# Performance work log

Hardware: AMD Instinct MI355X
Metric: run time of the kernel (lower is better)

The kernel has to match this reference:

```python
import jax, jax.numpy as jnp
import numpy as np

H, D = 8, 16          # heads, per-head dim (hidden_channels=128)
HID = H * D
N = 200000            # movie nodes
E = 500000            # edges per metapath relation
IN = 256              # input feature dim
CLS = 3               # output classes


def setup_inputs() -> dict:
    key = jax.random.key(0)
    ks = jax.random.split(key, 13)
    return {
        "x_movie": jax.random.normal(ks[0], (N, IN), jnp.float32),
        "W_proj": jax.random.normal(ks[1], (IN, HID), jnp.float32) * 0.05,
        "b_proj": jnp.zeros((HID,), jnp.float32),
        "att_src0": jax.random.normal(ks[2], (H, D), jnp.float32) * 0.1,
        "att_dst0": jax.random.normal(ks[3], (H, D), jnp.float32) * 0.1,
        "att_src1": jax.random.normal(ks[4], (H, D), jnp.float32) * 0.1,
        "att_dst1": jax.random.normal(ks[5], (H, D), jnp.float32) * 0.1,
        "q": jax.random.normal(ks[6], (HID,), jnp.float32) * 0.1,
        "k_w": jax.random.normal(ks[7], (HID, HID), jnp.float32) * 0.05,
        "k_b": jnp.zeros((HID,), jnp.float32),
        "lin_w": jax.random.normal(ks[8], (HID, CLS), jnp.float32) * 0.05,
        "lin_b": jnp.zeros((CLS,), jnp.float32),
        "e0_src": jax.random.randint(ks[9], (E,), 0, N, jnp.int32),
        "e0_dst": jax.random.randint(ks[10], (E,), 0, N, jnp.int32),
        "e1_src": jax.random.randint(ks[11], (E,), 0, N, jnp.int32),
        "e1_dst": jax.random.randint(ks[12], (E,), 0, N, jnp.int32),
    }


def _han_rel(h, att_s, att_d, src, dst, n):
    # h: [N, H, D]; GAT-style per-relation attention with segment softmax over dst
    a_s = jnp.sum(h * att_s, axis=-1)                      # [N, H]
    a_d = jnp.sum(h * att_d, axis=-1)                      # [N, H]
    alpha = jax.nn.leaky_relu(a_s[src] + a_d[dst], 0.2)    # [E, H]
    m = jax.ops.segment_max(alpha, dst, num_segments=n)    # per-dst max
    ex = jnp.exp(alpha - m[dst])
    den = jax.ops.segment_sum(ex, dst, num_segments=n)
    w = ex / (den[dst] + 1e-16)                            # edge softmax (PyG eps)
    msg = (h[src] * w[:, :, None]).reshape(-1, HID)        # [E, HID]
    return jax.nn.relu(jax.ops.segment_sum(msg, dst, num_segments=n))


def reference(x_movie, W_proj, b_proj, att_src0, att_dst0, att_src1, att_dst1,
              q, k_w, k_b, lin_w, lin_b, e0_src, e0_dst, e1_src, e1_dst):
    # node-type projection (HANConv.proj), dropout omitted (eval mode)
    h = (x_movie @ W_proj + b_proj).reshape(-1, H, D)      # [N, H, D]
    out0 = _han_rel(h, att_src0, att_dst0, e0_src, e0_dst, N)  # [N, HID]
    out1 = _han_rel(h, att_src1, att_dst1, e1_src, e1_dst, N)
    # semantic-level attention (HANConv.group)
    outs = jnp.stack([out0, out1])                         # [M=2, N, HID]
    score = jnp.sum(jnp.tanh(outs @ k_w + k_b).mean(axis=1) * q, axis=-1)  # [M]
    beta = jax.nn.softmax(score)
    fused = jnp.einsum('m,mnf->nf', beta, outs)            # [N, HID]
    return fused @ lin_w + lin_b                           # [N, CLS]
```

## Files before the change

kernel.cpp:

```cpp
#include <hip/hip_runtime.h>


typedef __attribute__((ext_vector_type(8))) short bf16x8;
typedef __attribute__((ext_vector_type(4))) float f32x4;
typedef __attribute__((ext_vector_type(8))) unsigned short ushort8;

__device__ __forceinline__ unsigned short f2b(float f) {
  union { float f; unsigned u; } v; v.f = f;
  unsigned r = v.u + 0x7fffu + ((v.u >> 16) & 1u);
  return (unsigned short)(r >> 16);
}
__device__ __forceinline__ float b2f(unsigned short u) {
  union { unsigned u; float f; } v; v.u = ((unsigned)u) << 16;
  return v.f;
}
__device__ __forceinline__ float fast_tanh(float x) {
  x = fminf(fmaxf(x, -15.f), 15.f);
  float t = __expf(2.f * x);
  return 1.f - 2.f / (t + 1.f);
}
__device__ __forceinline__ void gload_lds16(const void* g, void* l) {
  __builtin_amdgcn_global_load_lds(
      (const __attribute__((address_space(1))) unsigned int*)g,
      (__attribute__((address_space(3))) unsigned int*)l, 16, 0, 0);
}

__global__ __launch_bounds__(256) void prep_lite(
    const int* __restrict__ e0d, const int* __restrict__ e1d,
    int* __restrict__ deg, int ne, int n,
    const float* __restrict__ Wp, const float* __restrict__ kwm,
    unsigned short* __restrict__ Wpf, unsigned short* __restrict__ Kwf) {
  const int tid = threadIdx.x;
  int b = blockIdx.x;
  const int cb = (2 * ne + 255) >> 8;
  if (b < cb) {
    int e = b * 256 + tid;
    if (e < ne) atomicAdd(&deg[e0d[e]], 1);
    else if (e < 2 * ne) atomicAdd(&deg[n + e1d[e - ne]], 1);
    return;
  }
  b -= cb;
  int t = b * 256 + tid;
  const float* W; unsigned short* Wf; int idx;
  if (t < 4096) { W = Wp; Wf = Wpf; idx = t; }
  else if (t < 6144) { W = kwm; Wf = Kwf; idx = t - 4096; }
  else return;
  int lane = idx & 63, nt = (idx >> 6) & 7, kt = idx >> 9;
  int c = lane & 15, ks = lane >> 4;
  int kbase = kt * 32 + ks * 8;
  int col = nt * 16 + c;
  ushort8 o;
#pragma unroll
  for (int j = 0; j < 8; ++j) o[j] = f2b(W[(size_t)(kbase + j) * 128 + col]);
  *(ushort8*)(Wf + (size_t)idx * 8) = o;
}

__global__ __launch_bounds__(256) void proj_mfma(
    const float* __restrict__ X, const unsigned short* __restrict__ Wf,
    const float* __restrict__ bias,
    const float* __restrict__ as0v, const float* __restrict__ ad0v,
    const float* __restrict__ as1v, const float* __restrict__ ad1v,
    unsigned short* __restrict__ Hb, float* __restrict__ preb, int n) {
  __shared__ float buf[2][4096];
  const int tid = threadIdx.x;
  const int wid = tid >> 6, lane = tid & 63;
  const int wm = wid >> 1, wn = wid & 1;
  const int row0 = blockIdx.x * 64;
  const int r = lane & 15, ks = lane >> 4;

  f32x4 acc[2][4] = {};
  const unsigned short* bptr = Wf + ((size_t)(wn * 4) * 64 + lane) * 8;
  bf16x8 Br0[8], Br1[8];

#define VMWAIT(N) asm volatile("s_waitcnt vmcnt(" #N ")" ::: "memory")
#define SBAR()                                                                 \
  {                                                                            \
    __builtin_amdgcn_sched_barrier(0);                                         \
    __builtin_amdgcn_s_barrier();                                              \
    __builtin_amdgcn_sched_barrier(0);                                         \
  }

#define STAGE(b, s)                                                            \
  {                                                                            \
    _Pragma("unroll")                                                          \
    for (int i = 0; i < 4; ++i) {                                              \
      int rloc = wid * 16 + i * 4 + ks;                                        \
      int grow = row0 + rloc;                                                  \
      grow = grow < n ? grow : n - 1;                                          \
      const float* src =                                                       \
          X + (size_t)grow * 256 + (s) * 64 + ((r ^ (rloc & 7)) << 2);         \
      gload_lds16(src, &buf[b][(wid * 16 + i * 4) * 64]);                      \
    }                                                                          \
  }

#define BLOAD(P, s)                                                            \
  {                                                                            \
    _Pragma("unroll")                                                          \
    for (int j = 0; j < 8; ++j)                                                \
      P[j] = *(const bf16x8*)(bptr +                                           \
                (((size_t)(s) * 2 + (j >> 2)) * 8 + (j & 3)) * 512);           \
  }

#define COMPUTE_R(b, P)                                                        \
  {                                                                            \
    _Pragma("unroll")                                                          \
    for (int kt = 0; kt < 2; ++kt) {                                           \
      bf16x8 a[2];                                                             \
      _Pragma("unroll")                                                        \
      for (int mi = 0; mi < 2; ++mi) {                                         \
        int rr = wm * 32 + mi * 16 + r;                                        \
        const float* lrow = &buf[b][rr * 64];                                  \
        int c0 = kt * 8 + ks * 2;                                              \
        int sw = rr & 7;                                                       \
        float4 f0 = *(const float4*)(lrow + ((c0 ^ sw) * 4));                  \
        float4 f1 = *(const float4*)(lrow + (((c0 + 1) ^ sw) * 4));            \
        bf16x8 v;                                                              \
        v[0] = (short)f2b(f0.x); v[1] = (short)f2b(f0.y);                      \
        v[2] = (short)f2b(f0.z); v[3] = (short)f2b(f0.w);                      \
        v[4] = (short)f2b(f1.x); v[5] = (short)f2b(f1.y);                      \
        v[6] = (short)f2b(f1.z); v[7] = (short)f2b(f1.w);                      \
        a[mi] = v;                                                             \
      }                                                                        \
      _Pragma("unroll")                                                        \
      for (int ni = 0; ni < 4; ++ni) {                                         \
        acc[0][ni] = __builtin_amdgcn_mfma_f32_16x16x32_bf16(                  \
            a[0], P[kt * 4 + ni], acc[0][ni], 0, 0, 0);                        \
        acc[1][ni] = __builtin_amdgcn_mfma_f32_16x16x32_bf16(                  \
            a[1], P[kt * 4 + ni], acc[1][ni], 0, 0, 0);                        \
      }                                                                        \
    }                                                                          \
  }

  STAGE(0, 0);
  BLOAD(Br0, 0);
  STAGE(1, 1);
  VMWAIT(4); SBAR();
  BLOAD(Br1, 1);
  COMPUTE_R(0, Br0);
  SBAR();
  STAGE(0, 2);
  VMWAIT(4); SBAR();
  BLOAD(Br0, 2);
  COMPUTE_R(1, Br1);
  SBAR();
  STAGE(1, 3);
  VMWAIT(4); SBAR();
  BLOAD(Br1, 3);
  COMPUTE_R(0, Br0);
  SBAR();
  VMWAIT(0); SBAR();
  COMPUTE_R(1, Br1);
  __syncthreads();
#undef STAGE
#undef BLOAD
#undef COMPUTE_R
#undef VMWAIT
#undef SBAR

  unsigned short* ct = (unsigned short*)&buf[0][0];
#pragma unroll
  for (int ni = 0; ni < 4; ++ni) {
    const int col = wn * 64 + ni * 16 + r;
    const float bv = bias[col];
#pragma unroll
    for (int mi = 0; mi < 2; ++mi)
#pragma unroll
      for (int i = 0; i < 4; ++i)
        ct[(wm * 32 + mi * 16 + ks * 4 + i) * 136 + col] = f2b(acc[mi][ni][i] + bv);
  }
  __syncthreads();

  {
    int row = tid >> 2, qq = tid & 3;
    int grow = row0 + row;
    if (grow < n) {
      ushort8* dst = (ushort8*)(Hb + (size_t)grow * 128 + qq * 32);
#pragma unroll
      for (int j = 0; j < 4; ++j) dst[j] = *(ushort8*)&ct[row * 136 + qq * 32 + j * 8];
    }
  }

  const size_t n8 = (size_t)n * 8;
  for (int rh = tid; rh < 512; rh += 256) {
    int row = rh >> 3, head = rh & 7;
    int node = row0 + row;
    if (node < n) {
      float hv[16];
#pragma unroll
      for (int j = 0; j < 16; ++j) hv[j] = b2f(ct[row * 136 + head * 16 + j]);
      float s0 = 0, d0 = 0, s1 = 0, d1 = 0;
      const float* p0 = as0v + head * 16;
      const float* p1 = ad0v + head * 16;
      const float* p2 = as1v + head * 16;
      const float* p3 = ad1v + head * 16;
#pragma unroll
      for (int j = 0; j < 16; ++j) {
        float v = hv[j];
        s0 += v * p0[j]; d0 += v * p1[j];
        s1 += v * p2[j]; d1 += v * p3[j];
      }
      size_t idx = (size_t)node * 8 + head;
      preb[idx] = s0;
      preb[n8 + idx] = d0;
      preb[2 * n8 + idx] = s1;
      preb[3 * n8 + idx] = d1;
    }
  }
}

__global__ __launch_bounds__(256) void scan1_kernel(
    const int* __restrict__ deg, int* __restrict__ pre, int* __restrict__ bsum, int m) {
  __shared__ int sd[256];
  int t = threadIdx.x;
  int base = blockIdx.x * 2048 + t * 8;
  int v[8], sum = 0;
#pragma unroll
  for (int j = 0; j < 8; ++j) {
    v[j] = (base + j < m) ? deg[base + j] : 0;
    sum += v[j];
  }
  sd[t] = sum;
  __syncthreads();
  for (int off = 1; off < 256; off <<= 1) {
    int x = (t >= off) ? sd[t - off] : 0;
    __syncthreads();
    if (t >= off) sd[t] += x;
    __syncthreads();
  }
  if (t == 255) bsum[blockIdx.x] = sd[255];
  int run = sd[t] - sum;
#pragma unroll
  for (int j = 0; j < 8; ++j) {
    if (base + j < m) pre[base + j] = run;
    run += v[j];
  }
}

__global__ __launch_bounds__(256) void scan2_kernel(int* __restrict__ bsum, int nb) {
  __shared__ int sd[256];
  int t = threadIdx.x;
  int v = (t < nb) ? bsum[t] : 0;
  sd[t] = v;
  __syncthreads();
  for (int off = 1; off < 256; off <<= 1) {
    int x = (t >= off) ? sd[t - off] : 0;
    __syncthreads();
    if (t >= off) sd[t] += x;
    __syncthreads();
  }
  if (t < nb) bsum[t] = sd[t] - v;
}

__global__ void scan3_kernel(int* __restrict__ pre, const int* __restrict__ bsum, int m, int total) {
  int i = blockIdx.x * 256 + threadIdx.x;
  if (i < m) pre[i] += bsum[i >> 11];
  if (i == m) pre[m] = total;
}

__global__ void fill2_kernel(const int* __restrict__ e0s, const int* __restrict__ e0d,
                             const int* __restrict__ e1s, const int* __restrict__ e1d,
                             const int* __restrict__ pre, int* __restrict__ cur,
                             int* __restrict__ csr, int ne, int n) {
  int e = blockIdx.x * 256 + threadIdx.x;
  int s, idx;
  if (e < ne) { idx = e0d[e]; s = e0s[e]; }
  else if (e < 2 * ne) { idx = n + e1d[e - ne]; s = e1s[e - ne]; }
  else return;
  int slot = pre[idx] + atomicAdd(&cur[idx], 1);
  csr[slot] = s;
}

__global__ __launch_bounds__(512) void aggscore_mfma(
    const int* __restrict__ pre, const int* __restrict__ csr,
    const unsigned short* __restrict__ Hb, const float* __restrict__ preb,
    const unsigned short* __restrict__ Kf, const float* __restrict__ kb,
    const float* __restrict__ q, const float* __restrict__ lw,
    float* __restrict__ pout, float* __restrict__ sb, int n) {
  __shared__ unsigned short at[16384];
  __shared__ float red[8];
  const int rel = blockIdx.y;
  const int tid = threadIdx.x;
  const int row0 = blockIdx.x * 128;
  const size_t n8 = (size_t)n * 8;
  const float* a_s = preb + (size_t)(2 * rel) * n8;
  const float* a_d = preb + (size_t)(2 * rel + 1) * n8;

  {
    const int lane8 = tid & 7;
    const int nsub = tid >> 3;
#pragma unroll
    for (int it = 0; it < 2; ++it) {
      int row = it * 64 + nsub;
      int node = row0 + row;
      float s = 0.f;
      float acc[16] = {};
      if (node < n) {
        int beg = pre[rel * n + node];
        int cnt = pre[rel * n + node + 1] - beg;
        if (cnt > 0) {
          float ad = a_d[(size_t)node * 8 + lane8];
          int i0 = csr[beg];
          int i1 = csr[beg + (cnt > 1 ? 1 : 0)];
          float as0 = a_s[(size_t)i0 * 8 + lane8];
          float as1 = a_s[(size_t)i1 * 8 + lane8];
          const ushort8* hp0 = (const ushort8*)(Hb + (size_t)i0 * 128 + lane8 * 16);
          const ushort8* hp1 = (const ushort8*)(Hb + (size_t)i1 * 128 + lane8 * 16);
          ushort8 h0a = hp0[0], h0b = hp0[1];
          ushort8 h1a = hp1[0], h1b = hp1[1];
          for (int k = 0; k < cnt; k += 2) {
            int c2 = (k + 2 < cnt) ? k + 2 : cnt - 1;
            int c3 = (k + 3 < cnt) ? k + 3 : cnt - 1;
            int j0 = csr[beg + c2], j1 = csr[beg + c3];
            float nas0 = a_s[(size_t)j0 * 8 + lane8];
            float nas1 = a_s[(size_t)j1 * 8 + lane8];
            const ushort8* np0 = (const ushort8*)(Hb + (size_t)j0 * 128 + lane8 * 16);
            const ushort8* np1 = (const ushort8*)(Hb + (size_t)j1 * 128 + lane8 * 16);
            ushort8 nh0a = np0[0], nh0b = np0[1];
            ushort8 nh1a = np1[0], nh1b = np1[1];
            float al0 = as0 + ad, al1 = as1 + ad;
            al0 = (al0 >= 0.f) ? al0 : 0.2f * al0;
            al1 = (al1 >= 0.f) ? al1 : 0.2f * al1;
            float p0 = __expf(al0);
            float p1 = (k + 1 < cnt) ? __expf(al1) : 0.f;
            s += p0 + p1;
#pragma unroll
            for (int j = 0; j < 8; ++j) {
              acc[j]     += p0 * b2f(h0a[j]) + p1 * b2f(h1a[j]);
              acc[8 + j] += p0 * b2f(h0b[j]) + p1 * b2f(h1b[j]);
            }
            as0 = nas0; as1 = nas1;
            h0a = nh0a; h0b = nh0b; h1a = nh1a; h1b = nh1b;
          }
        }
      }
      float inv = 1.f / (s + 1e-16f);
      ushort8 o0, o1;
#pragma unroll
      for (int j = 0; j < 8; ++j) {
        o0[j] = f2b(fmaxf(acc[j] * inv, 0.f));
        o1[j] = f2b(fmaxf(acc[8 + j] * inv, 0.f));
      }
      int sw = row & 7;
      *(ushort8*)&at[row * 128 + (((lane8 * 2) ^ sw) * 8)] = o0;
      *(ushort8*)&at[row * 128 + (((lane8 * 2 + 1) ^ sw) * 8)] = o1;
    }
  }
  __syncthreads();

  const int wid = tid >> 6;
  float part = 0.f;
  if (wid < 4) {
    const int lane = tid & 63;
    const int wm = wid >> 1, wn = wid & 1;
    const int r = lane & 15, ks = lane >> 4;
    f32x4 acc[4][4] = {};
    const unsigned short* bptr = Kf + ((size_t)(wn * 4) * 64 + lane) * 8;
    __builtin_amdgcn_s_setprio(1);
#pragma unroll
    for (int kt = 0; kt < 4; ++kt) {
      bf16x8 a[4], b[4];
#pragma unroll
      for (int mi = 0; mi < 4; ++mi) {
        int row = wm * 64 + mi * 16 + r;
        a[mi] = *(const bf16x8*)&at[row * 128 + (((kt * 4 + ks) ^ (row & 7)) * 8)];
      }
#pragma unroll
      for (int ni = 0; ni < 4; ++ni)
        b[ni] = *(const bf16x8*)(bptr + ((size_t)kt * 8 + ni) * 512);
#pragma unroll
      for (int mi = 0; mi < 4; ++mi)
#pragma unroll
        for (int ni = 0; ni < 4; ++ni)
          acc[mi][ni] = __builtin_amdgcn_mfma_f32_16x16x32_bf16(a[mi], b[ni], acc[mi][ni], 0, 0, 0);
    }
    __builtin_amdgcn_s_setprio(0);
#pragma unroll
    for (int ni = 0; ni < 4; ++ni) {
      const int col = wn * 64 + ni * 16 + r;
      const float kbv = kb[col], qv = q[col];
#pragma unroll
      for (int mi = 0; mi < 4; ++mi) {
#pragma unroll
        for (int i = 0; i < 4; ++i) {
          int row = row0 + wm * 64 + mi * 16 + ks * 4 + i;
          if (row < n) part += fast_tanh(acc[mi][ni][i] + kbv) * qv;
        }
      }
    }
  } else if (tid < 384) {
    int t2 = tid - 256;
    int node = row0 + t2;
    if (node < n) {
      float p0 = 0.f, p1 = 0.f, p2 = 0.f;
      int s = t2 & 7;
#pragma unroll
      for (int c = 0; c < 16; ++c) {
        const unsigned short* rp = &at[t2 * 128 + ((c ^ s) * 8)];
#pragma unroll
        for (int j = 0; j < 8; ++j) {
          float v = b2f(rp[j]);
          const float* w = lw + (size_t)(c * 8 + j) * 3;
          p0 += v * w[0]; p1 += v * w[1]; p2 += v * w[2];
        }
      }
      float4 o = make_float4(p0, p1, p2, 0.f);
      *(float4*)(pout + (size_t)node * 8 + rel * 4) = o;
    }
  }
#pragma unroll
  for (int off = 32; off > 0; off >>= 1) part += __shfl_down(part, off, 64);
  if ((tid & 63) == 0) red[wid] = part;
  __syncthreads();
  if (tid == 0) {
    float t = 0.f;
#pragma unroll
    for (int w = 0; w < 8; ++w) t += red[w];
    atomicAdd(&sb[rel], t);
  }
}

__global__ __launch_bounds__(256) void final3_kernel(
    const float* __restrict__ pout, const float* __restrict__ sb,
    const float* __restrict__ lb, float* __restrict__ out, int n, float invn) {
  int node = blockIdx.x * 256 + threadIdx.x;
  if (node >= n) return;
  float s0 = sb[0] * invn, s1 = sb[1] * invn;
  float m = fmaxf(s0, s1);
  float e0 = __expf(s0 - m), e1 = __expf(s1 - m);
  float d = e0 + e1;
  float b0 = e0 / d, b1 = e1 / d;
  const float4* p = (const float4*)(pout + (size_t)node * 8);
  float4 pa = p[0], pb = p[1];
  float* dd = out + (size_t)node * 3;
  dd[0] = b0 * pa.x + b1 * pb.x + lb[0];
  dd[1] = b0 * pa.y + b1 * pb.y + lb[1];
  dd[2] = b0 * pa.z + b1 * pb.z + lb[2];
}

extern "C" void kernel_launch(void* const* d_in, const int* in_sizes, int n_in,
                              void* d_out, int out_size, void* d_ws, size_t ws_size,
                              hipStream_t stream) {
  const float* x   = (const float*)d_in[0];
  const float* Wp  = (const float*)d_in[1];
  const float* bp  = (const float*)d_in[2];
  const float* as0 = (const float*)d_in[3];
  const float* ad0 = (const float*)d_in[4];
  const float* as1 = (const float*)d_in[5];
  const float* ad1 = (const float*)d_in[6];
  const float* q   = (const float*)d_in[7];
  const float* kw  = (const float*)d_in[8];
  const float* kb  = (const float*)d_in[9];
  const float* lw  = (const float*)d_in[10];
  const float* lb  = (const float*)d_in[11];
  const int* e0s = (const int*)d_in[12];
  const int* e0d = (const int*)d_in[13];
  const int* e1s = (const int*)d_in[14];
  const int* e1d = (const int*)d_in[15];
  const int n  = in_sizes[0] / 256;
  const int ne = in_sizes[12];
  float* out = (float*)d_out;

  char* ws = (char*)d_ws;
  size_t off = 0;
  auto alloc = [&](size_t b) -> char* {
    char* p = ws + off;
    off = (off + b + 255) & ~(size_t)255;
    return p;
  };
  unsigned short* h    = (unsigned short*)alloc((size_t)n * 128 * 2);
  float* preb = (float*)alloc((size_t)4 * n * 8 * 4);
  float* pout = (float*)alloc((size_t)n * 8 * 4);
  int* pre    = (int*)alloc((size_t)(2 * n + 1) * 4);
  int* csr    = (int*)alloc((size_t)2 * ne * 4);
  int* deg    = (int*)alloc(((size_t)4 * n + 4) * 4);
  int* cur    = deg + 2 * n;
  float* sb   = (float*)(deg + 4 * n);
  int* bsum   = (int*)alloc(256 * 4);
  unsigned short* Wpf = (unsigned short*)alloc((size_t)4096 * 8 * 2);
  unsigned short* Kwf = (unsigned short*)alloc((size_t)2048 * 8 * 2);

  const int m = 2 * n;
  const int nblk_scan = (m + 2047) / 2048;
  const int cnt_blks = (2 * ne + 255) / 256;

  hipMemsetAsync(deg, 0, ((size_t)4 * n + 4) * 4, stream);
  hipLaunchKernelGGL(prep_lite, dim3(cnt_blks + 24), dim3(256), 0, stream,
                     e0d, e1d, deg, ne, n, Wp, kw, Wpf, Kwf);

  const int gproj = (n + 63) / 64;
  hipLaunchKernelGGL(proj_mfma, dim3(gproj), dim3(256), 0, stream,
                     x, Wpf, bp, as0, ad0, as1, ad1, h, preb, n);

  hipLaunchKernelGGL(scan1_kernel, dim3(nblk_scan), dim3(256), 0, stream, deg, pre, bsum, m);
  hipLaunchKernelGGL(scan2_kernel, dim3(1), dim3(256), 0, stream, bsum, nblk_scan);
  hipLaunchKernelGGL(scan3_kernel, dim3((m + 1 + 255) / 256), dim3(256), 0, stream,
                     pre, bsum, m, 2 * ne);
  hipLaunchKernelGGL(fill2_kernel, dim3((2 * ne + 255) / 256), dim3(256), 0, stream,
                     e0s, e0d, e1s, e1d, pre, cur, csr, ne, n);

  hipLaunchKernelGGL(aggscore_mfma, dim3((n + 127) / 128, 2), dim3(512), 0, stream,
                     pre, csr, h, preb, Kwf, kb, q, lw, pout, sb, n);
  hipLaunchKernelGGL(final3_kernel, dim3((n + 255) / 256), dim3(256), 0, stream,
                     pout, sb, lb, out, n, 1.0f / n);
}
```

Measured before the change: 295.9 us.

## Sort destination nodes by in-degree bucket to balance aggregation work

After: 355.7 us. 1.2x slower.

```diff
diff --git a/kernel.cpp b/kernel.cpp
--- a/kernel.cpp
+++ b/kernel.cpp
@@ -53,6 +53,70 @@
 #pragma unroll
   for (int j = 0; j < 8; ++j) o[j] = f2b(W[(size_t)(kbase + j) * 128 + col]);
   *(ushort8*)(Wf + (size_t)idx * 8) = o;
+}
+
+#define NBIN 66
+__global__ __launch_bounds__(256) void hist1_kernel(
+    const int* __restrict__ deg, int* __restrict__ hist2d, int m, int n) {
+  __shared__ int lh[NBIN];
+  int tid = threadIdx.x;
+  if (tid < NBIN) lh[tid] = 0;
+  __syncthreads();
+  int base = blockIdx.x * 2048 + tid * 8;
+#pragma unroll
+  for (int j = 0; j < 8; ++j) {
+    int i = base + j;
+    if (i < m) {
+      int d = deg[i]; d = d < 32 ? d : 32;
+      atomicAdd(&lh[(i >= n ? 33 : 0) + d], 1);
+    }
+  }
+  __syncthreads();
+  if (tid < NBIN) hist2d[blockIdx.x * NBIN + tid] = lh[tid];
+}
+
+__global__ __launch_bounds__(128) void hist2_kernel(int* __restrict__ hist2d, int nb) {
+  __shared__ int tot[NBIN];
+  __shared__ int bb[NBIN];
+  int t = threadIdx.x;
+  if (t < NBIN) {
+    int run = 0;
+    for (int b = 0; b < nb; ++b) {
+      int v = hist2d[b * NBIN + t];
+      hist2d[b * NBIN + t] = run;
+      run += v;
+    }
+    tot[t] = run;
+  }
+  __syncthreads();
+  if (t == 0) {
+    int base = 0;
+    for (int j = 0; j < NBIN; ++j) { bb[j] = base; base += tot[j]; }
+  }
+  __syncthreads();
+  if (t < NBIN) {
+    int add = bb[t];
+    for (int b = 0; b < nb; ++b) hist2d[b * NBIN + t] += add;
+  }
+}
+
+__global__ __launch_bounds__(256) void scat_kernel(
+    const int* __restrict__ deg, const int* __restrict__ hist2d,
+    int* __restrict__ order, int m, int n) {
+  __shared__ int lcur[NBIN];
+  int tid = threadIdx.x;
+  if (tid < NBIN) lcur[tid] = hist2d[blockIdx.x * NBIN + tid];
+  __syncthreads();
+  int base = blockIdx.x * 2048 + tid * 8;
+#pragma unroll
+  for (int j = 0; j < 8; ++j) {
+    int i = base + j;
+    if (i < m) {
+      int d = deg[i]; d = d < 32 ? d : 32;
+      int pos = atomicAdd(&lcur[(i >= n ? 33 : 0) + d], 1);
+      order[pos] = i;
+    }
+  }
 }
 
 __global__ __launch_bounds__(256) void proj_mfma(
@@ -271,19 +335,19 @@
 }
 
 __global__ __launch_bounds__(512) void aggscore_mfma(
-    const int* __restrict__ pre, const int* __restrict__ csr,
-    const unsigned short* __restrict__ Hb, const float* __restrict__ preb,
-    const unsigned short* __restrict__ Kf, const float* __restrict__ kb,
-    const float* __restrict__ q, const float* __restrict__ lw,
-    float* __restrict__ pout, float* __restrict__ sb, int n) {
+    const int* __restrict__ order, const int* __restrict__ pre,
+    const int* __restrict__ csr, const unsigned short* __restrict__ Hb,
+    const float* __restrict__ preb, const unsigned short* __restrict__ Kf,
+    const float* __restrict__ kb, const float* __restrict__ q,
+    const float* __restrict__ lw, float* __restrict__ pout,
+    float* __restrict__ sb, int n) {
   __shared__ unsigned short at[16384];
-  __shared__ float red[8];
-  const int rel = blockIdx.y;
+  __shared__ unsigned char relw[128];
+  __shared__ float red[2][8];
   const int tid = threadIdx.x;
-  const int row0 = blockIdx.x * 128;
+  const int g0 = blockIdx.x * 128;
   const size_t n8 = (size_t)n * 8;
-  const float* a_s = preb + (size_t)(2 * rel) * n8;
-  const float* a_d = preb + (size_t)(2 * rel + 1) * n8;
+  const int m = 2 * n;
 
   {
     const int lane8 = tid & 7;
@@ -291,12 +355,18 @@
 #pragma unroll
     for (int it = 0; it < 2; ++it) {
       int row = it * 64 + nsub;
-      int node = row0 + row;
+      int g = g0 + row;
       float s = 0.f;
       float acc[16] = {};
-      if (node < n) {
-        int beg = pre[rel * n + node];
-        int cnt = pre[rel * n + node + 1] - beg;
+      if (g < m) {
+        int idx = order[g];
+        int rel = idx >= n ? 1 : 0;
+        int node = idx - rel * n;
+        if (lane8 == 0) relw[row] = (unsigned char)rel;
+        const float* a_s = preb + (size_t)(2 * rel) * n8;
+        const float* a_d = preb + (size_t)(2 * rel + 1) * n8;
+        int beg = pre[idx];
+        int cnt = pre[idx + 1] - beg;
         if (cnt > 0) {
           float ad = a_d[(size_t)node * 8 + lane8];
           int i0 = csr[beg];
@@ -332,6 +402,8 @@
             h0a = nh0a; h0b = nh0b; h1a = nh1a; h1b = nh1b;
           }
         }
+      } else if (lane8 == 0) {
+        relw[row] = 0;
       }
       float inv = 1.f / (s + 1e-16f);
       ushort8 o0, o1;
@@ -348,7 +420,7 @@
   __syncthreads();
 
   const int wid = tid >> 6;
-  float part = 0.f;
+  float part0 = 0.f, part1 = 0.f;
   if (wid < 4) {
     const int lane = tid & 63;
     const int wm = wid >> 1, wn = wid & 1;
@@ -382,15 +454,21 @@
       for (int mi = 0; mi < 4; ++mi) {
 #pragma unroll
         for (int i = 0; i < 4; ++i) {
-          int row = row0 + wm * 64 + mi * 16 + ks * 4 + i;
-          if (row < n) part += fast_tanh(acc[mi][ni][i] + kbv) * qv;
+          int row = wm * 64 + mi * 16 + ks * 4 + i;
+          if (g0 + row < m) {
+            float v = fast_tanh(acc[mi][ni][i] + kbv) * qv;
+            if (relw[row]) part1 += v; else part0 += v;
+          }
         }
       }
     }
   } else if (tid < 384) {
     int t2 = tid - 256;
-    int node = row0 + t2;
-    if (node < n) {
+    int g = g0 + t2;
+    if (g < m) {
+      int idx = order[g];
+      int rel = idx >= n ? 1 : 0;
+      int node = idx - rel * n;
       float p0 = 0.f, p1 = 0.f, p2 = 0.f;
       int s = t2 & 7;
 #pragma unroll
@@ -408,14 +486,18 @@
     }
   }
 #pragma unroll
-  for (int off = 32; off > 0; off >>= 1) part += __shfl_down(part, off, 64);
-  if ((tid & 63) == 0) red[wid] = part;
+  for (int off = 32; off > 0; off >>= 1) {
+    part0 += __shfl_down(part0, off, 64);
+    part1 += __shfl_down(part1, off, 64);
+  }
+  if ((tid & 63) == 0) { red[0][wid] = part0; red[1][wid] = part1; }
   __syncthreads();
   if (tid == 0) {
-    float t = 0.f;
-#pragma unroll
-    for (int w = 0; w < 8; ++w) t += red[w];
-    atomicAdd(&sb[rel], t);
+    float t0 = 0.f, t1 = 0.f;
+#pragma unroll
+    for (int w = 0; w < 8; ++w) { t0 += red[0][w]; t1 += red[1][w]; }
+    if (t0 != 0.f) atomicAdd(&sb[0], t0);
+    if (t1 != 0.f) atomicAdd(&sb[1], t1);
   }
 }
 
@@ -467,11 +549,16 @@
     off = (off + b + 255) & ~(size_t)255;
     return p;
   };
+  const int m = 2 * n;
+  const int nbh = (m + 2047) / 2048;
+
   unsigned short* h    = (unsigned short*)alloc((size_t)n * 128 * 2);
   float* preb = (float*)alloc((size_t)4 * n * 8 * 4);
   float* pout = (float*)alloc((size_t)n * 8 * 4);
-  int* pre    = (int*)alloc((size_t)(2 * n + 1) * 4);
+  int* pre    = (int*)alloc((size_t)(m + 1) * 4);
   int* csr    = (int*)alloc((size_t)2 * ne * 4);
+  int* order  = (int*)alloc((size_t)m * 4);
+  int* hist2d = (int*)alloc((size_t)nbh * NBIN * 4);
   int* deg    = (int*)alloc(((size_t)4 * n + 4) * 4);
   int* cur    = deg + 2 * n;
   float* sb   = (float*)(deg + 4 * n);
@@ -479,7 +566,6 @@
   unsigned short* Wpf = (unsigned short*)alloc((size_t)4096 * 8 * 2);
   unsigned short* Kwf = (unsigned short*)alloc((size_t)2048 * 8 * 2);
 
-  const int m = 2 * n;
   const int nblk_scan = (m + 2047) / 2048;
   const int cnt_blks = (2 * ne + 255) / 256;
 
@@ -490,6 +576,10 @@
   const int gproj = (n + 63) / 64;
   hipLaunchKernelGGL(proj_mfma, dim3(gproj), dim3(256), 0, stream,
                      x, Wpf, bp, as0, ad0, as1, ad1, h, preb, n);
+
+  hipLaunchKernelGGL(hist1_kernel, dim3(nbh), dim3(256), 0, stream, deg, hist2d, m, n);
+  hipLaunchKernelGGL(hist2_kernel, dim3(1), dim3(128), 0, stream, hist2d, nbh);
+  hipLaunchKernelGGL(scat_kernel, dim3(nbh), dim3(256), 0, stream, deg, hist2d, order, m, n);
 
   hipLaunchKernelGGL(scan1_kernel, dim3(nblk_scan), dim3(256), 0, stream, deg, pre, bsum, m);
   hipLaunchKernelGGL(scan2_kernel, dim3(1), dim3(256), 0, stream, bsum, nblk_scan);
@@ -498,8 +588,8 @@
   hipLaunchKernelGGL(fill2_kernel, dim3((2 * ne + 255) / 256), dim3(256), 0, stream,
                      e0s, e0d, e1s, e1d, pre, cur, csr, ne, n);
 
-  hipLaunchKernelGGL(aggscore_mfma, dim3((n + 127) / 128, 2), dim3(512), 0, stream,
-                     pre, csr, h, preb, Kwf, kb, q, lw, pout, sb, n);
+  hipLaunchKernelGGL(aggscore_mfma, dim3((m + 127) / 128), dim3(512), 0, stream,
+                     order, pre, csr, h, preb, Kwf, kb, q, lw, pout, sb, n);
   hipLaunchKernelGGL(final3_kernel, dim3((n + 255) / 256), dim3(256), 0, stream,
                      pout, sb, lb, out, n, 1.0f / n);
 }
```
